# Optimization experiments

Measured on AMD Instinct MI355X. Metric: run time of the kernel, lower is better.

Reference implementation:

```python
import jax, jax.numpy as jnp
import numpy as np

N_QUBITS = 4
N_LAYERS = 3
BATCH = 1000000


def _apply_1q(state, m00, m01, m10, m11, q):
    # state: [B, 2,2,2,2]; apply 2x2 gate on qubit axis q (broadcastable m's)
    s = jnp.moveaxis(state, q + 1, 1)
    a0, a1 = s[:, 0], s[:, 1]
    out = jnp.stack([m00 * a0 + m01 * a1, m10 * a0 + m11 * a1], axis=1)
    return jnp.moveaxis(out, 1, q + 1)


def _rx(state, theta, q):
    # PennyLane RX: [[cos(t/2), -i sin(t/2)], [-i sin(t/2), cos(t/2)]]; theta is per-batch [B]
    h = theta * 0.5
    sh = (-1,) + (1,) * (N_QUBITS - 1)  # broadcast over remaining qubit axes
    c = jnp.cos(h).reshape(sh)
    s = jnp.sin(h).reshape(sh)
    return _apply_1q(state, c, -1j * s, -1j * s, c, q)


def _ry(state, theta, q):
    # PennyLane RY: [[cos, -sin], [sin, cos]] of t/2; theta is a shared scalar
    h = theta * 0.5
    c = jnp.cos(h)
    s = jnp.sin(h)
    return _apply_1q(state, c, -s, s, c, q)


def _cnot(state, ctrl, tgt):
    # ctrl < tgt in the ladder; flip target amplitudes where control bit == 1
    s = jnp.moveaxis(state, ctrl + 1, 1)
    s = jnp.moveaxis(s, tgt + 1, 2)
    s = jnp.concatenate([s[:, :1], s[:, 1:, ::-1]], axis=1)
    s = jnp.moveaxis(s, 2, tgt + 1)
    return jnp.moveaxis(s, 1, ctrl + 1)


def _expval_z(probs, w):
    pm = jnp.moveaxis(probs, w + 1, 1)
    pm = pm.reshape(pm.shape[0], 2, -1)
    return pm[:, 0].sum(-1) - pm[:, 1].sum(-1)


def _circuit(angles, weights):
    # angles: [B, n_qubits]; weights: [n_layers, n_qubits]
    B = angles.shape[0]
    state = jnp.zeros((B,) + (2,) * N_QUBITS, jnp.complex64)
    state = state.at[(slice(None),) + (0,) * N_QUBITS].set(1.0)
    for layer in range(N_LAYERS):
        for i in range(N_QUBITS):
            state = _rx(state, angles[:, i], i)
        for i in range(N_QUBITS):
            state = _ry(state, weights[layer, i], i)
        for i in range(N_QUBITS - 1):
            state = _cnot(state, i, i + 1)
    probs = jnp.real(state * jnp.conj(state))
    return jnp.stack([_expval_z(probs, 0), _expval_z(probs, 1)], axis=-1)  # [B, 2]


def setup_inputs() -> dict:
    key = jax.random.key(0)
    k1, k2 = jax.random.split(key)
    x = jax.random.normal(k1, (BATCH, N_QUBITS), dtype=jnp.float32)
    weights = jax.random.uniform(k2, (N_LAYERS, N_QUBITS), dtype=jnp.float32,
                                 minval=0.0, maxval=2.0 * np.pi)
    w_input = jnp.ones((N_QUBITS,), jnp.float32)
    w_output = jnp.full((2,), 50.0, jnp.float32)
    return {"x": x, "w_input": w_input, "weights": weights, "w_output": w_output}


def reference(x, w_input, weights, w_output):
    angles = jnp.arctan(x * w_input)          # input scaling + atan embedding
    out = _circuit(angles, weights)           # [B, 2] PauliZ expvals in [-1, 1]
    return (1.0 + out) / 2.0 * w_output       # rescale to [0, w_output]
```

## Files before the change

### kernel.cpp

```cpp
#include <hip/hip_runtime.h>


__device__ __forceinline__ float rdlane(float x, int l) {
    return __int_as_float(__builtin_amdgcn_readlane(__float_as_int(x), l));
}

__device__ __forceinline__ void rx_p(float (&re)[16], float (&im)[16],
                                     float c, float s,
                                     const int (&lo)[8], const int (&hi)[8]) {
#pragma unroll
    for (int t = 0; t < 8; ++t) {
        const int i = lo[t], j = hi[t];
        float a0r = re[i], a0i = im[i], a1r = re[j], a1i = im[j];
        re[i] = __builtin_fmaf(c, a0r,  s * a1i);
        im[i] = __builtin_fmaf(c, a0i, -(s * a1r));
        re[j] = __builtin_fmaf(c, a1r,  s * a0i);
        im[j] = __builtin_fmaf(c, a1i, -(s * a0r));
    }
}

__device__ __forceinline__ void ry_p(float (&re)[16], float (&im)[16],
                                     float c, float s,
                                     const int (&lo)[8], const int (&hi)[8]) {
#pragma unroll
    for (int t = 0; t < 8; ++t) {
        const int i = lo[t], j = hi[t];
        float a0r = re[i], a0i = im[i], a1r = re[j], a1i = im[j];
        re[i] = __builtin_fmaf(c, a0r, -(s * a1r));
        im[i] = __builtin_fmaf(c, a0i, -(s * a1i));
        re[j] = __builtin_fmaf(s, a0r,   c * a1r);
        im[j] = __builtin_fmaf(s, a0i,   c * a1i);
    }
}

__global__ __launch_bounds__(256) void heaq_kernel(
    const float4* __restrict__ x4,
    const float*  __restrict__ w_input,
    const float*  __restrict__ weights,
    const float*  __restrict__ w_output,
    float2*       __restrict__ out2,
    int B)
{
    const int lane = threadIdx.x & 63;

    const float K = 0.07957747154594767f;
    float wv  = weights[lane < 12 ? lane : 0];
    float rev = __builtin_amdgcn_fractf(wv * K);
    float sn  = __builtin_amdgcn_sinf(rev);
    float cn  = __builtin_amdgcn_cosf(rev);

    const float cy0 = rdlane(cn, 0), sy0 = rdlane(sn, 0);
    const float cy1 = rdlane(cn, 1), sy1 = rdlane(sn, 1);
    const float cy2 = rdlane(cn, 2), sy2 = rdlane(sn, 2);
    const float cy3 = rdlane(cn, 3), sy3 = rdlane(sn, 3);
    const float cy4 = rdlane(cn, 4), sy4 = rdlane(sn, 4);
    const float cy5 = rdlane(cn, 5), sy5 = rdlane(sn, 5);
    const float cy6 = rdlane(cn, 6), sy6 = rdlane(sn, 6);
    const float cy8 = rdlane(cn, 8), sy8 = rdlane(sn, 8);
    const float cy9 = rdlane(cn, 9), sy9 = rdlane(sn, 9);

    const int b = blockIdx.x * 256 + threadIdx.x;
    if (b >= B) return;

    float4 xv = x4[b];
    float xs[4] = {xv.x, xv.y, xv.z, xv.w};
    float cx[4], sx[4];
#pragma unroll
    for (int q = 0; q < 4; ++q) {
        float u = xs[q] * w_input[q];
        float r = __builtin_amdgcn_rsqf(__builtin_fmaf(u, u, 1.0f));
        float c = __builtin_amdgcn_sqrtf(__builtin_fmaf(0.5f, r, 0.5f));
        cx[q] = c;
        sx[q] = 0.5f * u * r * __builtin_amdgcn_rcpf(c);
    }

    const float cys[4] = {cy0, cy1, cy2, cy3};
    const float sys[4] = {sy0, sy1, sy2, sy3};
    float vr[4][2], vi[4][2];
#pragma unroll
    for (int q = 0; q < 4; ++q) {
        vr[q][0] = cys[q] * cx[q];
        vi[q][0] = sys[q] * sx[q];
        vr[q][1] = sys[q] * cx[q];
        vi[q][1] = -cys[q] * sx[q];
    }
    float p2r[4], p2i[4];
#pragma unroll
    for (int i = 0; i < 4; ++i) {
        const int a = i >> 1, c = i & 1;
        p2r[i] = __builtin_fmaf(vr[0][a], vr[1][c], -(vi[0][a] * vi[1][c]));
        p2i[i] = __builtin_fmaf(vr[0][a], vi[1][c],   vi[0][a] * vr[1][c]);
    }
    float p3r[8], p3i[8];
#pragma unroll
    for (int i = 0; i < 8; ++i) {
        const int h = i >> 1, c = i & 1;
        p3r[i] = __builtin_fmaf(p2r[h], vr[2][c], -(p2i[h] * vi[2][c]));
        p3i[i] = __builtin_fmaf(p2r[h], vi[2][c],   p2i[h] * vr[2][c]);
    }
    constexpr int J[16] = {0,1,3,2, 7,6,4,5, 15,14,12,13, 8,9,11,10};
    float re[16], im[16];
#pragma unroll
    for (int i = 0; i < 16; ++i) {
        const int h = i >> 1, c = i & 1;
        re[J[i]] = __builtin_fmaf(p3r[h], vr[3][c], -(p3i[h] * vi[3][c]));
        im[J[i]] = __builtin_fmaf(p3r[h], vi[3][c],   p3i[h] * vr[3][c]);
    }

    static constexpr int m8_lo[8]  = {0,1,2,3,4,5,6,7};
    static constexpr int m8_hi[8]  = {8,9,10,11,12,13,14,15};
    static constexpr int m4_lo[8]  = {0,1,2,3,8,9,10,11};
    static constexpr int m4_hi[8]  = {4,5,6,7,12,13,14,15};
    static constexpr int m2_lo[8]  = {0,1,4,5,8,9,12,13};
    static constexpr int m2_hi[8]  = {2,3,6,7,10,11,14,15};
    static constexpr int x12_lo[8] = {0,1,2,3,4,5,6,7};
    static constexpr int x12_hi[8] = {12,13,14,15,8,9,10,11};
    static constexpr int x6_lo[8]  = {0,1,2,3,12,13,14,15};
    static constexpr int x6_hi[8]  = {6,7,4,5,10,11,8,9};

    rx_p(re, im, cx[0], sx[0], m8_lo, m8_hi);
    rx_p(re, im, cx[1], sx[1], m4_lo, m4_hi);
    rx_p(re, im, cx[2], sx[2], m2_lo, m2_hi);
    ry_p(re, im, cy4, sy4, m8_lo, m8_hi);
    ry_p(re, im, cy5, sy5, m4_lo, m4_hi);
    ry_p(re, im, cy6, sy6, m2_lo, m2_hi);

    rx_p(re, im, cx[0], sx[0], x12_lo, x12_hi);
    rx_p(re, im, cx[1], sx[1], x6_lo,  x6_hi);
    ry_p(re, im, cy8, sy8, x12_lo, x12_hi);
    ry_p(re, im, cy9, sy9, x6_lo,  x6_hi);

    float p[16];
#pragma unroll
    for (int i = 0; i < 16; ++i)
        p[i] = __builtin_fmaf(re[i], re[i], im[i] * im[i]);
    float S0 = (p[0] + p[1]) + (p[2]  + p[3]);
    float S1 = (p[4] + p[5]) + (p[6]  + p[7]);
    float S2 = (p[8] + p[9]) + (p[10] + p[11]);
    float S3 = (p[12]+ p[13])+ (p[14] + p[15]);
    float z0 = (S0 + S1) - (S2 + S3);
    float z1 = (S0 + S2) - (S1 + S3);

    float hw0 = 0.5f * w_output[0], hw1 = 0.5f * w_output[1];
    out2[b] = make_float2(__builtin_fmaf(z0, hw0, hw0),
                          __builtin_fmaf(z1, hw1, hw1));
}

extern "C" void kernel_launch(void* const* d_in, const int* in_sizes, int n_in,
                              void* d_out, int out_size, void* d_ws, size_t ws_size,
                              hipStream_t stream) {
    const float* x        = (const float*)d_in[0];
    const float* w_input  = (const float*)d_in[1];
    const float* weights  = (const float*)d_in[2];
    const float* w_output = (const float*)d_in[3];
    float* out = (float*)d_out;

    const int B = in_sizes[0] / 4;

    heaq_kernel<<<(B + 255) / 256, 256, 0, stream>>>(
        (const float4*)x, w_input, weights, w_output, (float2*)out, B);
}
```

Before: 90.17 us.

## Process two batch elements per thread and split state by last qubit

Each thread now handles two batch elements (b and b+H), halving the grid, and the 16-amplitude state is split into two 8-amplitude halves indexed by the final qubit. The final qubit's gates only affect the marginal probabilities, so they are dropped from the propagation. This is meant to raise instruction-level parallelism and amortise the per-thread setup (weights trig, readlanes). For odd B the last element is never processed, and register pressure rises.

```diff
diff --git a/kernel.cpp b/kernel.cpp
--- a/kernel.cpp
+++ b/kernel.cpp
@@ -5,11 +5,11 @@
     return __int_as_float(__builtin_amdgcn_readlane(__float_as_int(x), l));
 }
 
-__device__ __forceinline__ void rx_p(float (&re)[16], float (&im)[16],
-                                     float c, float s,
-                                     const int (&lo)[8], const int (&hi)[8]) {
+__device__ __forceinline__ void rx8(float (&re)[8], float (&im)[8],
+                                    float c, float s,
+                                    const int (&lo)[4], const int (&hi)[4]) {
 #pragma unroll
-    for (int t = 0; t < 8; ++t) {
+    for (int t = 0; t < 4; ++t) {
         const int i = lo[t], j = hi[t];
         float a0r = re[i], a0i = im[i], a1r = re[j], a1i = im[j];
         re[i] = __builtin_fmaf(c, a0r,  s * a1i);
@@ -19,11 +19,11 @@
     }
 }
 
-__device__ __forceinline__ void ry_p(float (&re)[16], float (&im)[16],
-                                     float c, float s,
-                                     const int (&lo)[8], const int (&hi)[8]) {
+__device__ __forceinline__ void ry8(float (&re)[8], float (&im)[8],
+                                    float c, float s,
+                                    const int (&lo)[4], const int (&hi)[4]) {
 #pragma unroll
-    for (int t = 0; t < 8; ++t) {
+    for (int t = 0; t < 4; ++t) {
         const int i = lo[t], j = hi[t];
         float a0r = re[i], a0i = im[i], a1r = re[j], a1i = im[j];
         re[i] = __builtin_fmaf(c, a0r, -(s * a1r));
@@ -59,91 +59,119 @@
     const float cy8 = rdlane(cn, 8), sy8 = rdlane(sn, 8);
     const float cy9 = rdlane(cn, 9), sy9 = rdlane(sn, 9);
 
+    const int H = B >> 1;
     const int b = blockIdx.x * 256 + threadIdx.x;
-    if (b >= B) return;
+    if (b >= H) return;
 
-    float4 xv = x4[b];
-    float xs[4] = {xv.x, xv.y, xv.z, xv.w};
-    float cx[4], sx[4];
-#pragma unroll
-    for (int q = 0; q < 4; ++q) {
-        float u = xs[q] * w_input[q];
-        float r = __builtin_amdgcn_rsqf(__builtin_fmaf(u, u, 1.0f));
-        float c = __builtin_amdgcn_sqrtf(__builtin_fmaf(0.5f, r, 0.5f));
-        cx[q] = c;
-        sx[q] = 0.5f * u * r * __builtin_amdgcn_rcpf(c);
-    }
+    const float wi0 = w_input[0], wi1 = w_input[1];
+    const float wi2 = w_input[2], wi3 = w_input[3];
+    const float hw0 = 0.5f * w_output[0], hw1 = 0.5f * w_output[1];
+
+    static constexpr int m4_lo[4] = {0,1,2,3}, m4_hi[4] = {4,5,6,7};
+    static constexpr int m2_lo[4] = {0,1,4,5}, m2_hi[4] = {2,3,6,7};
+    static constexpr int m1_lo[4] = {0,2,4,6}, m1_hi[4] = {1,3,5,7};
+    static constexpr int x6_lo[4] = {0,1,2,3}, x6_hi[4] = {6,7,4,5};
+    static constexpr int x3_lo[4] = {0,1,6,7}, x3_hi[4] = {3,2,5,4};
+    static constexpr int hk[8] = {0,1,3,2,6,7,5,4};
 
     const float cys[4] = {cy0, cy1, cy2, cy3};
     const float sys[4] = {sy0, sy1, sy2, sy3};
-    float vr[4][2], vi[4][2];
+
+    float Ar[2][8], Ai[2][8], Br[2][8], Bi[2][8];
+    float cx[2][3], sx[2][3];
+
 #pragma unroll
-    for (int q = 0; q < 4; ++q) {
-        vr[q][0] = cys[q] * cx[q];
-        vi[q][0] = sys[q] * sx[q];
-        vr[q][1] = sys[q] * cx[q];
-        vi[q][1] = -cys[q] * sx[q];
-    }
-    float p2r[4], p2i[4];
+    for (int e = 0; e < 2; ++e) {
+        const float4 xv = x4[e ? b + H : b];
+        const float xs[4] = {xv.x * wi0, xv.y * wi1, xv.z * wi2, xv.w * wi3};
+
+        float cq[4], sq[4];
 #pragma unroll
-    for (int i = 0; i < 4; ++i) {
-        const int a = i >> 1, c = i & 1;
-        p2r[i] = __builtin_fmaf(vr[0][a], vr[1][c], -(vi[0][a] * vi[1][c]));
-        p2i[i] = __builtin_fmaf(vr[0][a], vi[1][c],   vi[0][a] * vr[1][c]);
-    }
-    float p3r[8], p3i[8];
+        for (int q = 0; q < 4; ++q) {
+            float u = xs[q];
+            float r = __builtin_amdgcn_rsqf(__builtin_fmaf(u, u, 1.0f));
+            float c = __builtin_amdgcn_sqrtf(__builtin_fmaf(0.5f, r, 0.5f));
+            cq[q] = c;
+            sq[q] = 0.5f * u * r * __builtin_amdgcn_rcpf(c);
+        }
 #pragma unroll
-    for (int i = 0; i < 8; ++i) {
-        const int h = i >> 1, c = i & 1;
-        p3r[i] = __builtin_fmaf(p2r[h], vr[2][c], -(p2i[h] * vi[2][c]));
-        p3i[i] = __builtin_fmaf(p2r[h], vi[2][c],   p2i[h] * vr[2][c]);
-    }
-    constexpr int J[16] = {0,1,3,2, 7,6,4,5, 15,14,12,13, 8,9,11,10};
-    float re[16], im[16];
+        for (int q = 0; q < 3; ++q) { cx[e][q] = cq[q]; sx[e][q] = sq[q]; }
+
+        float vr[4][2], vi[4][2];
 #pragma unroll
-    for (int i = 0; i < 16; ++i) {
-        const int h = i >> 1, c = i & 1;
-        re[J[i]] = __builtin_fmaf(p3r[h], vr[3][c], -(p3i[h] * vi[3][c]));
-        im[J[i]] = __builtin_fmaf(p3r[h], vi[3][c],   p3i[h] * vr[3][c]);
+        for (int q = 0; q < 4; ++q) {
+            vr[q][0] = cys[q] * cq[q];
+            vi[q][0] = sys[q] * sq[q];
+            vr[q][1] = sys[q] * cq[q];
+            vi[q][1] = -cys[q] * sq[q];
+        }
+        float p2r[4], p2i[4];
+#pragma unroll
+        for (int i = 0; i < 4; ++i) {
+            const int a = i >> 1, c = i & 1;
+            p2r[i] = __builtin_fmaf(vr[0][a], vr[1][c], -(vi[0][a] * vi[1][c]));
+            p2i[i] = __builtin_fmaf(vr[0][a], vi[1][c],   vi[0][a] * vr[1][c]);
+        }
+        float p3r[8], p3i[8];
+#pragma unroll
+        for (int i = 0; i < 8; ++i) {
+            const int h = i >> 1, c = i & 1;
+            p3r[i] = __builtin_fmaf(p2r[h], vr[2][c], -(p2i[h] * vi[2][c]));
+            p3i[i] = __builtin_fmaf(p2r[h], vi[2][c],   p2i[h] * vr[2][c]);
+        }
+#pragma unroll
+        for (int k = 0; k < 8; ++k) {
+            const int h = hk[k], ta = k & 1, tb = ta ^ 1;
+            Ar[e][k] = __builtin_fmaf(p3r[h], vr[3][ta], -(p3i[h] * vi[3][ta]));
+            Ai[e][k] = __builtin_fmaf(p3r[h], vi[3][ta],   p3i[h] * vr[3][ta]);
+            Br[e][k] = __builtin_fmaf(p3r[h], vr[3][tb], -(p3i[h] * vi[3][tb]));
+            Bi[e][k] = __builtin_fmaf(p3r[h], vi[3][tb],   p3i[h] * vr[3][tb]);
+        }
     }
 
-    static constexpr int m8_lo[8]  = {0,1,2,3,4,5,6,7};
-    static constexpr int m8_hi[8]  = {8,9,10,11,12,13,14,15};
-    static constexpr int m4_lo[8]  = {0,1,2,3,8,9,10,11};
-    static constexpr int m4_hi[8]  = {4,5,6,7,12,13,14,15};
-    static constexpr int m2_lo[8]  = {0,1,4,5,8,9,12,13};
-    static constexpr int m2_hi[8]  = {2,3,6,7,10,11,14,15};
-    static constexpr int x12_lo[8] = {0,1,2,3,4,5,6,7};
-    static constexpr int x12_hi[8] = {12,13,14,15,8,9,10,11};
-    static constexpr int x6_lo[8]  = {0,1,2,3,12,13,14,15};
-    static constexpr int x6_hi[8]  = {6,7,4,5,10,11,8,9};
+#pragma unroll
+    for (int e = 0; e < 2; ++e) {
+        rx8(Ar[e], Ai[e], cx[e][0], sx[e][0], m4_lo, m4_hi);
+        rx8(Br[e], Bi[e], cx[e][0], sx[e][0], m4_lo, m4_hi);
+        rx8(Ar[e], Ai[e], cx[e][1], sx[e][1], m2_lo, m2_hi);
+        rx8(Br[e], Bi[e], cx[e][1], sx[e][1], m2_lo, m2_hi);
+        rx8(Ar[e], Ai[e], cx[e][2], sx[e][2], m1_lo, m1_hi);
+        rx8(Br[e], Bi[e], cx[e][2], sx[e][2], m1_lo, m1_hi);
+        ry8(Ar[e], Ai[e], cy4, sy4, m4_lo, m4_hi);
+        ry8(Br[e], Bi[e], cy4, sy4, m4_lo, m4_hi);
+        ry8(Ar[e], Ai[e], cy5, sy5, m2_lo, m2_hi);
+        ry8(Br[e], Bi[e], cy5, sy5, m2_lo, m2_hi);
+        ry8(Ar[e], Ai[e], cy6, sy6, m1_lo, m1_hi);
+        ry8(Br[e], Bi[e], cy6, sy6, m1_lo, m1_hi);
 
-    rx_p(re, im, cx[0], sx[0], m8_lo, m8_hi);
-    rx_p(re, im, cx[1], sx[1], m4_lo, m4_hi);
-    rx_p(re, im, cx[2], sx[2], m2_lo, m2_hi);
-    ry_p(re, im, cy4, sy4, m8_lo, m8_hi);
-    ry_p(re, im, cy5, sy5, m4_lo, m4_hi);
-    ry_p(re, im, cy6, sy6, m2_lo, m2_hi);
+        rx8(Ar[e], Ai[e], cx[e][0], sx[e][0], x6_lo, x6_hi);
+        rx8(Br[e], Bi[e], cx[e][0], sx[e][0], x6_lo, x6_hi);
+        rx8(Ar[e], Ai[e], cx[e][1], sx[e][1], x3_lo, x3_hi);
+        rx8(Br[e], Bi[e], cx[e][1], sx[e][1], x3_lo, x3_hi);
+        ry8(Ar[e], Ai[e], cy8, sy8, x6_lo, x6_hi);
+        ry8(Br[e], Bi[e], cy8, sy8, x6_lo, x6_hi);
+        ry8(Ar[e], Ai[e], cy9, sy9, x3_lo, x3_hi);
+        ry8(Br[e], Bi[e], cy9, sy9, x3_lo, x3_hi);
+    }
 
-    rx_p(re, im, cx[0], sx[0], x12_lo, x12_hi);
-    rx_p(re, im, cx[1], sx[1], x6_lo,  x6_hi);
-    ry_p(re, im, cy8, sy8, x12_lo, x12_hi);
-    ry_p(re, im, cy9, sy9, x6_lo,  x6_hi);
-
-    float p[16];
 #pragma unroll
-    for (int i = 0; i < 16; ++i)
-        p[i] = __builtin_fmaf(re[i], re[i], im[i] * im[i]);
-    float S0 = (p[0] + p[1]) + (p[2]  + p[3]);
-    float S1 = (p[4] + p[5]) + (p[6]  + p[7]);
-    float S2 = (p[8] + p[9]) + (p[10] + p[11]);
-    float S3 = (p[12]+ p[13])+ (p[14] + p[15]);
-    float z0 = (S0 + S1) - (S2 + S3);
-    float z1 = (S0 + S2) - (S1 + S3);
-
-    float hw0 = 0.5f * w_output[0], hw1 = 0.5f * w_output[1];
-    out2[b] = make_float2(__builtin_fmaf(z0, hw0, hw0),
-                          __builtin_fmaf(z1, hw1, hw1));
+    for (int e = 0; e < 2; ++e) {
+        float pk[8];
+#pragma unroll
+        for (int k = 0; k < 8; ++k) {
+            float t = __builtin_fmaf(Ar[e][k], Ar[e][k], Ai[e][k] * Ai[e][k]);
+            t = __builtin_fmaf(Br[e][k], Br[e][k], t);
+            pk[k] = __builtin_fmaf(Bi[e][k], Bi[e][k], t);
+        }
+        float G0 = pk[0] + pk[1];
+        float G1 = pk[2] + pk[3];
+        float G2 = pk[4] + pk[5];
+        float G3 = pk[6] + pk[7];
+        float z0 = (G0 + G1) - (G2 + G3);
+        float z1 = (G0 + G2) - (G1 + G3);
+        out2[e ? b + H : b] = make_float2(__builtin_fmaf(z0, hw0, hw0),
+                                          __builtin_fmaf(z1, hw1, hw1));
+    }
 }
 
 extern "C" void kernel_launch(void* const* d_in, const int* in_sizes, int n_in,
@@ -156,7 +184,8 @@
     float* out = (float*)d_out;
 
     const int B = in_sizes[0] / 4;
+    const int H = B >> 1;
 
-    heaq_kernel<<<(B + 255) / 256, 256, 0, stream>>>(
+    heaq_kernel<<<(H + 255) / 256, 256, 0, stream>>>(
         (const float4*)x, w_input, weights, w_output, (float2*)out, B);
 }
```

Result: no change. 90.99 us (+0.9%).
